# Kernel tuning notes

Measured on AMD Instinct MI355X. Metric: run time of the kernel, lower is better.

The kernel has to match this reference:

```python
import jax, jax.numpy as jnp
import numpy as np

B, S, D, H = 8, 1024, 768, 12
DH = D // H
EPS = 1e-5
NEG = -1e9


def _layernorm(x, g, b):
    mu = jnp.mean(x, axis=-1, keepdims=True)
    var = jnp.mean((x - mu) ** 2, axis=-1, keepdims=True)
    return (x - mu) * jax.lax.rsqrt(var + EPS) * g + b


def setup_inputs() -> dict:
    key = jax.random.key(0)
    ks = jax.random.split(key, 20)
    sc = 0.02
    x = jax.random.normal(ks[0], (B, S, D), dtype=jnp.float32)
    src_mask = jax.random.randint(ks[1], (B, S), 0, 2) > 0
    # weights stored as (in, out): y = x @ W + b (same math as torch x @ W.T + b)
    Wq = jax.random.normal(ks[2], (D, D), jnp.float32) * sc
    bq = jnp.zeros((D,), jnp.float32)
    Wk = jax.random.normal(ks[3], (D, D), jnp.float32) * sc
    bk = jnp.zeros((D,), jnp.float32)
    Wv = jax.random.normal(ks[4], (D, D), jnp.float32) * sc
    bv = jnp.zeros((D,), jnp.float32)
    Wo = jax.random.normal(ks[5], (D, D), jnp.float32) * sc
    bo = jnp.zeros((D,), jnp.float32)
    g1 = jnp.ones((D,), jnp.float32)
    be1 = jnp.zeros((D,), jnp.float32)
    W1 = jax.random.normal(ks[6], (D, 2 * D), jnp.float32) * sc
    b1 = jnp.zeros((2 * D,), jnp.float32)
    W2 = jax.random.normal(ks[7], (2 * D, D), jnp.float32) * sc
    b2 = jnp.zeros((D,), jnp.float32)
    g2 = jnp.ones((D,), jnp.float32)
    be2 = jnp.zeros((D,), jnp.float32)
    return dict(x=x, src_mask=src_mask, Wq=Wq, bq=bq, Wk=Wk, bk=bk, Wv=Wv, bv=bv,
                Wo=Wo, bo=bo, g1=g1, be1=be1, W1=W1, b1=b1, W2=W2, b2=b2,
                g2=g2, be2=be2)


def reference(x, src_mask, Wq, bq, Wk, bk, Wv, bv, Wo, bo, g1, be1, W1, b1, W2, b2, g2, be2):
    # QKV projections, split into heads: [B, S, H, DH]
    q = (x @ Wq + bq).reshape(B, S, H, DH)
    k = (x @ Wk + bk).reshape(B, S, H, DH)
    v = (x @ Wv + bv).reshape(B, S, H, DH)
    # scores [B, H, S, S]; scale by sqrt(head_dim) as in original
    scores = jnp.einsum('bqhd,bkhd->bhqk', q, k) / np.sqrt(DH).astype(np.float32)
    # additive key mask broadcast over heads and queries
    mask = jnp.where(src_mask[:, None, None, :], 0.0, NEG).astype(scores.dtype)
    A = jax.nn.softmax(scores + mask, axis=-1)
    ctx = jnp.einsum('bhqk,bkhd->bqhd', A, v).reshape(B, S, D)
    attn_out = ctx @ Wo + bo + x
    h = _layernorm(attn_out, g1, be1)
    ff = jax.nn.relu(h @ W1 + b1) @ W2 + b2
    out = _layernorm(ff + h, g2, be2)
    return out
```

## Files before the change

kernel.cpp:

```cpp
#include <hip/hip_runtime.h>
#include <cstdint>
#include <cstddef>

typedef unsigned short u16;
typedef __attribute__((ext_vector_type(8))) __bf16 bf16x8;
typedef __attribute__((ext_vector_type(4))) float floatx4;

#define Bz 8
#define Sz 1024
#define Dz 768
#define Hz 12
#define DHz 64

__device__ __forceinline__ u16 f2b(float f) {
  unsigned u = __float_as_uint(f);
  return (u16)((u + 0x7fffu + ((u >> 16) & 1u)) >> 16);
}

__device__ __forceinline__ bf16x8 ld8(const u16* p) {
  union { uint4 u; bf16x8 b; } t;
  t.u = *reinterpret_cast<const uint4*>(p);
  return t.b;
}

__device__ __forceinline__ void load_lds16(const u16* g, u16* l) {
  __builtin_amdgcn_global_load_lds(
      (const __attribute__((address_space(1))) unsigned int*)g,
      (__attribute__((address_space(3))) unsigned int*)l, 16, 0, 0);
}

__global__ __launch_bounds__(256) void cvt4(const float* __restrict__ src,
                                            u16* __restrict__ dst, int n4) {
  int i = blockIdx.x * 256 + threadIdx.x;
  if (i >= n4) return;
  float4 v = reinterpret_cast<const float4*>(src)[i];
  union { u16 s[4]; uint2 u; } t;
  t.s[0] = f2b(v.x); t.s[1] = f2b(v.y); t.s[2] = f2b(v.z); t.s[3] = f2b(v.w);
  reinterpret_cast<uint2*>(dst)[i] = t.u;
}

__global__ __launch_bounds__(256)
void wtrans(const float* __restrict__ s0, const float* __restrict__ s1,
            const float* __restrict__ s2, u16* __restrict__ dst,
            int K, int N, int srcN) {
  __shared__ float T[32][33];
  const int tx = threadIdx.x & 31, ty = threadIdx.x >> 5;
  const int n0 = blockIdx.x * 32, k0 = blockIdx.y * 32;
  const int n = n0 + tx;
  const float* src = s0;
  int nn = n;
  if (s1 && n >= 1536) { src = s2; nn = n - 1536; }
  else if (s1 && n >= 768) { src = s1; nn = n - 768; }
#pragma unroll
  for (int i = 0; i < 4; ++i)
    T[ty + i * 8][tx] = src[(size_t)(k0 + ty + i * 8) * srcN + nn];
  __syncthreads();
#pragma unroll
  for (int i = 0; i < 4; ++i)
    dst[(size_t)(n0 + ty + i * 8) * K + k0 + tx] = f2b(T[tx][ty + i * 8]);
}

template <int EPI>
__global__ __launch_bounds__(256, 3)
void gemm_k(const u16* __restrict__ A, const u16* __restrict__ Bt,
            int M, int N, int K,
            const float* __restrict__ bias0, const float* __restrict__ bias1,
            const float* __restrict__ bias2, const float* __restrict__ resid,
            float* __restrict__ outF, u16* __restrict__ outB,
            u16* __restrict__ qO, u16* __restrict__ kO, u16* __restrict__ vtO) {
  __shared__ __align__(16) u16 As[3][128 * 32];
  __shared__ __align__(16) u16 Bs[3][128 * 32];
  const int tid = threadIdx.x;
  const int lane = tid & 63, wave = tid >> 6;
  const int l15 = lane & 15, quad = lane >> 4;

  const int nx = gridDim.x;
  const int nwg = nx * gridDim.y;
  const int lin = blockIdx.y * nx + blockIdx.x;
  const int swz = (lin & 7) * (nwg >> 3) + (lin >> 3);
  const int bx = swz % nx, by = swz / nx;

  const int m0 = by * 128, n0 = bx * 128;
  const int wm = (wave >> 1) * 64, wn = (wave & 1) * 64;

  floatx4 acc[4][4];
#pragma unroll
  for (int i = 0; i < 4; ++i)
#pragma unroll
    for (int j = 0; j < 4; ++j) acc[i][j] = {0.f, 0.f, 0.f, 0.f};

  const int srow = lane >> 2;
  const int scol = (((lane & 3) ^ ((lane >> 3) & 3))) * 8;
  const u16* pA = A + (size_t)(m0 + wave * 32 + srow) * K + scol;
  const u16* pB = Bt + (size_t)(n0 + wave * 32 + srow) * K + scol;

#pragma unroll
  for (int t = 0; t < 2; ++t)
#pragma unroll
    for (int j = 0; j < 2; ++j) {
      load_lds16(pA + (size_t)(j * 16) * K + t * 32, &As[t][(wave * 2 + j) * 512]);
      load_lds16(pB + (size_t)(j * 16) * K + t * 32, &Bs[t][(wave * 2 + j) * 512]);
    }

  const int NIT = K >> 5;
  const int rsw = (l15 >> 1) & 3;
  int cur = 0;
  for (int i = 0; i < NIT; ++i) {
    if (i == NIT - 1) asm volatile("s_waitcnt vmcnt(0)" ::: "memory");
    else              asm volatile("s_waitcnt vmcnt(4)" ::: "memory");
    __builtin_amdgcn_s_barrier();
    bf16x8 af[4], bf[4];
#pragma unroll
    for (int ii = 0; ii < 4; ++ii)
      af[ii] = ld8(&As[cur][(wm + ii * 16 + l15) * 32 + (quad ^ rsw) * 8]);
#pragma unroll
    for (int j = 0; j < 4; ++j)
      bf[j] = ld8(&Bs[cur][(wn + j * 16 + l15) * 32 + (quad ^ rsw) * 8]);
    __builtin_amdgcn_sched_barrier(0);
    if (i + 2 < NIT) {
      const int k2 = (i + 2) << 5;
      int pf = cur + 2; if (pf >= 3) pf -= 3;
#pragma unroll
      for (int j = 0; j < 2; ++j) {
        load_lds16(pA + (size_t)(j * 16) * K + k2, &As[pf][(wave * 2 + j) * 512]);
        load_lds16(pB + (size_t)(j * 16) * K + k2, &Bs[pf][(wave * 2 + j) * 512]);
      }
    }
    __builtin_amdgcn_sched_barrier(0);
#pragma unroll
    for (int ii = 0; ii < 4; ++ii)
#pragma unroll
      for (int j = 0; j < 4; ++j)
        acc[ii][j] = __builtin_amdgcn_mfma_f32_16x16x32_bf16(af[ii], bf[j],
                                                             acc[ii][j], 0, 0, 0);
    cur += 1; if (cur == 3) cur = 0;
  }

#pragma unroll
  for (int i = 0; i < 4; ++i) {
    int mbase = m0 + wm + i * 16 + quad * 4;
#pragma unroll
    for (int j = 0; j < 4; ++j) {
      int n = n0 + wn + j * 16 + l15;
#pragma unroll
      for (int r = 0; r < 4; ++r) {
        int mm = mbase + r;
        float v = acc[i][j][r];
        if (EPI == 0) {
          if (n < 768) {
            v += bias0[n];
            qO[(size_t)mm * 768 + n] = f2b(v);
          } else if (n < 1536) {
            v += bias1[n - 768];
            kO[(size_t)mm * 768 + (n - 768)] = f2b(v);
          } else {
            int d = n - 1536;
            v += bias2[d];
            int hh = d >> 6, dh = d & 63;
            int bb = mm >> 10, ss = mm & 1023;
            vtO[((size_t)(bb * Hz + hh) * DHz + dh) * Sz + ss] = f2b(v);
          }
        } else if (EPI == 1) {
          v += bias0[n] + resid[(size_t)mm * N + n];
          outF[(size_t)mm * N + n] = v;
        } else {
          v += bias0[n];
          v = fmaxf(v, 0.f);
          outB[(size_t)mm * N + n] = f2b(v);
        }
      }
    }
  }
}

__global__ __launch_bounds__(256, 3)
void attn_k(const u16* __restrict__ q, const u16* __restrict__ kbuf,
            const u16* __restrict__ vt, const int* __restrict__ mask,
            u16* __restrict__ ctx) {
  __shared__ float addend[Sz];
  __shared__ __align__(16) u16 Ks[128 * 64];
  __shared__ __align__(16) u16 Vs[64 * 128];
  __shared__ __align__(16) u16 P[4][16][132];
  const int tid = threadIdx.x;
  const int wave = tid >> 6, lane = tid & 63;
  const int l15 = lane & 15, quad = lane >> 4;
  const int lin = blockIdx.y * 16 + blockIdx.x;
  const int swzid = (lin & 7) * 192 + (lin >> 3);
  const int bq = swzid & 15;
  const int bh = swzid >> 4;
  const int b = bh / Hz, h = bh - b * Hz;

  for (int s = tid; s < Sz; s += 256)
    addend[s] = mask[b * Sz + s] ? 0.f : -1e9f;

  const int qrow = bq * 64 + wave * 16 + l15;
  const u16* qp = q + (size_t)(b * Sz + qrow) * Dz + h * DHz;
  const bf16x8 fq0 = ld8(qp + quad * 8);
  const bf16x8 fq1 = ld8(qp + 32 + quad * 8);

  const int kchunk = (lane & 7) ^ (lane >> 3);
  const int l7 = l15 & 7;
  const int s0q = quad ^ l7;

  float m_l = -1e30f, l_l = 0.f;
  floatx4 o[4];
#pragma unroll
  for (int nt = 0; nt < 4; ++nt) o[nt] = {0.f, 0.f, 0.f, 0.f};

  const size_t vbase = (size_t)(b * Hz + h) * DHz * Sz;

  for (int kt = 0; kt < Sz / 128; ++kt) {
    __syncthreads();
#pragma unroll
    for (int j = 0; j < 4; ++j) {
      const int key = wave * 32 + j * 8 + (lane >> 3);
      load_lds16(kbuf + (size_t)(b * Sz + kt * 128 + key) * Dz + h * DHz +
                     kchunk * 8,
                 Ks + wave * 2048 + j * 512);
      const int dh = wave * 16 + j * 4 + (lane >> 4);
      const int vchunk = (lane & 15) ^ (dh & 7);
      load_lds16(vt + vbase + (size_t)dh * Sz + kt * 128 + vchunk * 8,
                 Vs + wave * 2048 + j * 512);
    }
    __syncthreads();

    floatx4 z[8];
#pragma unroll
    for (int t = 0; t < 8; ++t) {
      const int krow = t * 16 + l15;
      bf16x8 fk0 = ld8(&Ks[krow * 64 + s0q * 8]);
      bf16x8 fk1 = ld8(&Ks[krow * 64 + (s0q ^ 4) * 8]);
      floatx4 zz = {0.f, 0.f, 0.f, 0.f};
      zz = __builtin_amdgcn_mfma_f32_16x16x32_bf16(fk0, fq0, zz, 0, 0, 0);
      zz = __builtin_amdgcn_mfma_f32_16x16x32_bf16(fk1, fq1, zz, 0, 0, 0);
      const float4 ad =
          *reinterpret_cast<const float4*>(&addend[kt * 128 + t * 16 + quad * 4]);
      z[t][0] = zz[0] * 0.125f + ad.x;
      z[t][1] = zz[1] * 0.125f + ad.y;
      z[t][2] = zz[2] * 0.125f + ad.z;
      z[t][3] = zz[3] * 0.125f + ad.w;
    }
    float mx = z[0][0];
#pragma unroll
    for (int t = 0; t < 8; ++t)
#pragma unroll
      for (int r = 0; r < 4; ++r) mx = fmaxf(mx, z[t][r]);
    mx = fmaxf(mx, __shfl_xor(mx, 16, 64));
    mx = fmaxf(mx, __shfl_xor(mx, 32, 64));
    const float nm = fmaxf(m_l, mx);
    const float alpha = __expf(m_l - nm);
    m_l = nm;
    float su = 0.f;
#pragma unroll
    for (int t = 0; t < 8; ++t) {
      union { u16 s[4]; uint2 u; } pk;
#pragma unroll
      for (int r = 0; r < 4; ++r) {
        float p = __expf(z[t][r] - nm);
        su += p;
        pk.s[r] = f2b(p);
      }
      *reinterpret_cast<uint2*>(&P[wave][l15][t * 16 + quad * 4]) = pk.u;
    }
    su += __shfl_xor(su, 16, 64);
    su += __shfl_xor(su, 32, 64);
    l_l = l_l * alpha + su;
    float av[4];
#pragma unroll
    for (int r = 0; r < 4; ++r) av[r] = __shfl(alpha, quad * 4 + r, 64);
#pragma unroll
    for (int nt = 0; nt < 4; ++nt)
#pragma unroll
      for (int r = 0; r < 4; ++r) o[nt][r] *= av[r];
    bf16x8 ap[4];
#pragma unroll
    for (int c = 0; c < 4; ++c)
      ap[c] = ld8(&P[wave][l15][c * 32 + quad * 8]);
#pragma unroll
    for (int nt = 0; nt < 4; ++nt) {
#pragma unroll
      for (int c = 0; c < 4; ++c) {
        bf16x8 bv =
            ld8(&Vs[(nt * 16 + l15) * 128 + (((c * 4 + quad) ^ l7) * 8)]);
        o[nt] = __builtin_amdgcn_mfma_f32_16x16x32_bf16(ap[c], bv, o[nt], 0, 0, 0);
      }
    }
  }

  const float linv = 1.f / l_l;
  float lv[4];
#pragma unroll
  for (int r = 0; r < 4; ++r) lv[r] = __shfl(linv, quad * 4 + r, 64);
  const int qr = bq * 64 + wave * 16 + quad * 4;
#pragma unroll
  for (int nt = 0; nt < 4; ++nt)
#pragma unroll
    for (int r = 0; r < 4; ++r) {
      float v = o[nt][r] * lv[r];
      ctx[(size_t)(b * Sz + qr + r) * Dz + h * DHz + nt * 16 + l15] = f2b(v);
    }
}

__global__ __launch_bounds__(256)
void ln_k(const float* __restrict__ in, const float* __restrict__ g,
          const float* __restrict__ be, float* __restrict__ outF,
          u16* __restrict__ outB) {
  const int row = blockIdx.x;
  const float* x = in + (size_t)row * Dz;
  const int tid = threadIdx.x;
  float v0 = x[tid], v1 = x[tid + 256], v2 = x[tid + 512];
  float s = v0 + v1 + v2;
  float s2 = v0 * v0 + v1 * v1 + v2 * v2;
#pragma unroll
  for (int off = 1; off < 64; off <<= 1) {
    s += __shfl_xor(s, off, 64);
    s2 += __shfl_xor(s2, off, 64);
  }
  __shared__ float red[8];
  int wave = tid >> 6, lane = tid & 63;
  if (lane == 0) { red[wave] = s; red[4 + wave] = s2; }
  __syncthreads();
  s = red[0] + red[1] + red[2] + red[3];
  s2 = red[4] + red[5] + red[6] + red[7];
  const float mu = s * (1.f / 768.f);
  const float rstd = rsqrtf(s2 * (1.f / 768.f) - mu * mu + 1e-5f);
  float vv[3] = {v0, v1, v2};
#pragma unroll
  for (int e = 0; e < 3; ++e) {
    int col = tid + e * 256;
    float y = (vv[e] - mu) * rstd * g[col] + be[col];
    outF[(size_t)row * Dz + col] = y;
    if (outB) outB[(size_t)row * Dz + col] = f2b(y);
  }
}

extern "C" void kernel_launch(void* const* d_in, const int* in_sizes, int n_in,
                              void* d_out, int out_size, void* d_ws,
                              size_t ws_size, hipStream_t stream) {
  const float* x   = (const float*)d_in[0];
  const int*   msk = (const int*)d_in[1];
  const float* Wq  = (const float*)d_in[2];
  const float* bq  = (const float*)d_in[3];
  const float* Wk  = (const float*)d_in[4];
  const float* bk  = (const float*)d_in[5];
  const float* Wv  = (const float*)d_in[6];
  const float* bv  = (const float*)d_in[7];
  const float* Wo  = (const float*)d_in[8];
  const float* bo  = (const float*)d_in[9];
  const float* g1  = (const float*)d_in[10];
  const float* be1 = (const float*)d_in[11];
  const float* W1  = (const float*)d_in[12];
  const float* b1  = (const float*)d_in[13];
  const float* W2  = (const float*)d_in[14];
  const float* b2  = (const float*)d_in[15];
  const float* g2  = (const float*)d_in[16];
  const float* be2 = (const float*)d_in[17];
  float* out = (float*)d_out;

  char* ws = (char*)d_ws;
  u16*   xb    = (u16*)(ws + 0);
  u16*   wqkvb = (u16*)(ws + 12582912);
  u16*   wob   = (u16*)(ws + 16121856);
  u16*   w1b   = (u16*)(ws + 17301504);
  u16*   w2b   = (u16*)(ws + 19660800);
  u16*   qb    = (u16*)(ws + 22020096);
  u16*   kb    = (u16*)(ws + 34603008);
  u16*   vtb   = (u16*)(ws + 47185920);
  u16*   ctx   = (u16*)(ws + 59768832);
  float* att   = (float*)(ws + 72351744);
  float* hf    = (float*)(ws + 97517568);
  u16*   hb    = (u16*)(ws + 122683392);
  u16*   f1    = (u16*)(ws + 47185920);
  float* yy    = (float*)(ws + 22020096);

  cvt4<<<6291456 / 4 / 256, 256, 0, stream>>>(x, xb, 6291456 / 4);
  wtrans<<<dim3(2304 / 32, 768 / 32), 256, 0, stream>>>(Wq, Wk, Wv, wqkvb, 768,
                                                        2304, 768);
  wtrans<<<dim3(24, 24), 256, 0, stream>>>(Wo, nullptr, nullptr, wob, 768, 768,
                                           768);
  wtrans<<<dim3(48, 24), 256, 0, stream>>>(W1, nullptr, nullptr, w1b, 768, 1536,
                                           1536);
  wtrans<<<dim3(24, 48), 256, 0, stream>>>(W2, nullptr, nullptr, w2b, 1536, 768,
                                           768);

  gemm_k<0><<<dim3(2304 / 128, 8192 / 128), 256, 0, stream>>>(
      xb, wqkvb, 8192, 2304, 768, bq, bk, bv, nullptr, nullptr, nullptr, qb, kb,
      vtb);
  attn_k<<<dim3(Sz / 64, Bz * Hz), 256, 0, stream>>>(qb, kb, vtb, msk, ctx);
  gemm_k<1><<<dim3(768 / 128, 8192 / 128), 256, 0, stream>>>(
      ctx, wob, 8192, 768, 768, bo, nullptr, nullptr, x, att, nullptr, nullptr,
      nullptr, nullptr);
  ln_k<<<8192, 256, 0, stream>>>(att, g1, be1, hf, hb);
  gemm_k<2><<<dim3(1536 / 128, 8192 / 128), 256, 0, stream>>>(
      hb, w1b, 8192, 1536, 768, b1, nullptr, nullptr, nullptr, nullptr, f1,
      nullptr, nullptr, nullptr);
  gemm_k<1><<<dim3(768 / 128, 8192 / 128), 256, 0, stream>>>(
      f1, w2b, 8192, 768, 1536, b2, nullptr, nullptr, hf, yy, nullptr, nullptr,
      nullptr, nullptr);
  ln_k<<<8192, 256, 0, stream>>>(yy, g2, be2, out, nullptr);
}
```

Measured before the change: 368.8 us.

## Double-buffer K/V tiles in attention with lazy softmax rescaling

The attention kernel now uses 64-key tiles with double-buffered LDS for K and V. The next tile is prefetched with global_load_lds while the current one is computed, and a single barrier is used per iteration. The online softmax rescale is skipped unless the running max grows by more than a threshold, and the probabilities are packed to bf16 with the hardware conversion. This aims to hide global load latency and cut exp/shuffle/rescale work, at the cost of more loop iterations, reliance on manual vmcnt waits, and possible precision drift from the lazy max.

Result: faster. 357.8 us (-3.0%).

```diff
diff --git a/kernel.cpp b/kernel.cpp
--- a/kernel.cpp
+++ b/kernel.cpp
@@ -15,6 +15,11 @@
 __device__ __forceinline__ u16 f2b(float f) {
   unsigned u = __float_as_uint(f);
   return (u16)((u + 0x7fffu + ((u >> 16) & 1u)) >> 16);
+}
+
+__device__ __forceinline__ u16 f2b_hw(float f) {
+  __bf16 h = (__bf16)f;
+  return __builtin_bit_cast(u16, h);
 }
 
 __device__ __forceinline__ bf16x8 ld8(const u16* p) {
@@ -178,9 +183,9 @@
             const u16* __restrict__ vt, const int* __restrict__ mask,
             u16* __restrict__ ctx) {
   __shared__ float addend[Sz];
-  __shared__ __align__(16) u16 Ks[128 * 64];
-  __shared__ __align__(16) u16 Vs[64 * 128];
-  __shared__ __align__(16) u16 P[4][16][132];
+  __shared__ __align__(16) u16 Ks[2][64 * 64];
+  __shared__ __align__(16) u16 Vs[2][64 * 64];
+  __shared__ __align__(16) u16 P[4][16][68];
   const int tid = threadIdx.x;
   const int wave = tid >> 6, lane = tid & 63;
   const int l15 = lane & 15, quad = lane >> 4;
@@ -198,92 +203,104 @@
   const bf16x8 fq0 = ld8(qp + quad * 8);
   const bf16x8 fq1 = ld8(qp + 32 + quad * 8);
 
-  const int kchunk = (lane & 7) ^ (lane >> 3);
   const int l7 = l15 & 7;
   const int s0q = quad ^ l7;
 
+  const int srow = tid >> 3;
+  const int spos = tid & 7;
+  const int schunk = spos ^ (srow & 7);
+  const u16* kg = kbuf + (size_t)(b * Sz + srow) * Dz + h * DHz + schunk * 8;
+  const u16* vg = vt + (size_t)(b * Hz + h) * (DHz * Sz) + (size_t)srow * Sz +
+                  schunk * 8;
+
   float m_l = -1e30f, l_l = 0.f;
   floatx4 o[4];
 #pragma unroll
   for (int nt = 0; nt < 4; ++nt) o[nt] = {0.f, 0.f, 0.f, 0.f};
 
-  const size_t vbase = (size_t)(b * Hz + h) * DHz * Sz;
-
-  for (int kt = 0; kt < Sz / 128; ++kt) {
-    __syncthreads();
-#pragma unroll
-    for (int j = 0; j < 4; ++j) {
-      const int key = wave * 32 + j * 8 + (lane >> 3);
-      load_lds16(kbuf + (size_t)(b * Sz + kt * 128 + key) * Dz + h * DHz +
-                     kchunk * 8,
-                 Ks + wave * 2048 + j * 512);
-      const int dh = wave * 16 + j * 4 + (lane >> 4);
-      const int vchunk = (lane & 15) ^ (dh & 7);
-      load_lds16(vt + vbase + (size_t)dh * Sz + kt * 128 + vchunk * 8,
-                 Vs + wave * 2048 + j * 512);
-    }
-    __syncthreads();
-
-    floatx4 z[8];
-#pragma unroll
-    for (int t = 0; t < 8; ++t) {
+  load_lds16(kg, &Ks[0][wave * 512]);
+  load_lds16(kg + (size_t)32 * Dz, &Ks[0][2048 + wave * 512]);
+  load_lds16(vg, &Vs[0][wave * 512]);
+  load_lds16(vg + (size_t)32 * Sz, &Vs[0][2048 + wave * 512]);
+
+  for (int kt = 0; kt < 16; ++kt) {
+    const int cur = kt & 1;
+    asm volatile("s_waitcnt vmcnt(0)" ::: "memory");
+    __builtin_amdgcn_s_barrier();
+    bf16x8 fk0[4], fk1[4];
+#pragma unroll
+    for (int t = 0; t < 4; ++t) {
       const int krow = t * 16 + l15;
-      bf16x8 fk0 = ld8(&Ks[krow * 64 + s0q * 8]);
-      bf16x8 fk1 = ld8(&Ks[krow * 64 + (s0q ^ 4) * 8]);
+      fk0[t] = ld8(&Ks[cur][krow * 64 + s0q * 8]);
+      fk1[t] = ld8(&Ks[cur][krow * 64 + (s0q ^ 4) * 8]);
+    }
+    __builtin_amdgcn_sched_barrier(0);
+    if (kt + 1 < 16) {
+      const size_t ko = (size_t)(kt + 1) * 64 * Dz;
+      const int ve = (kt + 1) * 64;
+      const int nb = cur ^ 1;
+      load_lds16(kg + ko, &Ks[nb][wave * 512]);
+      load_lds16(kg + ko + (size_t)32 * Dz, &Ks[nb][2048 + wave * 512]);
+      load_lds16(vg + ve, &Vs[nb][wave * 512]);
+      load_lds16(vg + ve + (size_t)32 * Sz, &Vs[nb][2048 + wave * 512]);
+    }
+    __builtin_amdgcn_sched_barrier(0);
+
+    floatx4 z[4];
+#pragma unroll
+    for (int t = 0; t < 4; ++t) {
       floatx4 zz = {0.f, 0.f, 0.f, 0.f};
-      zz = __builtin_amdgcn_mfma_f32_16x16x32_bf16(fk0, fq0, zz, 0, 0, 0);
-      zz = __builtin_amdgcn_mfma_f32_16x16x32_bf16(fk1, fq1, zz, 0, 0, 0);
+      zz = __builtin_amdgcn_mfma_f32_16x16x32_bf16(fk0[t], fq0, zz, 0, 0, 0);
+      zz = __builtin_amdgcn_mfma_f32_16x16x32_bf16(fk1[t], fq1, zz, 0, 0, 0);
       const float4 ad =
-          *reinterpret_cast<const float4*>(&addend[kt * 128 + t * 16 + quad * 4]);
+          *reinterpret_cast<const float4*>(&addend[kt * 64 + t * 16 + quad * 4]);
       z[t][0] = zz[0] * 0.125f + ad.x;
       z[t][1] = zz[1] * 0.125f + ad.y;
       z[t][2] = zz[2] * 0.125f + ad.z;
       z[t][3] = zz[3] * 0.125f + ad.w;
     }
-    float mx = z[0][0];
-#pragma unroll
-    for (int t = 0; t < 8; ++t)
-#pragma unroll
-      for (int r = 0; r < 4; ++r) mx = fmaxf(mx, z[t][r]);
+    float mx = fmaxf(fmaxf(z[0][0], z[0][1]), fmaxf(z[0][2], z[0][3]));
+#pragma unroll
+    for (int t = 1; t < 4; ++t)
+      mx = fmaxf(mx, fmaxf(fmaxf(z[t][0], z[t][1]), fmaxf(z[t][2], z[t][3])));
     mx = fmaxf(mx, __shfl_xor(mx, 16, 64));
     mx = fmaxf(mx, __shfl_xor(mx, 32, 64));
-    const float nm = fmaxf(m_l, mx);
-    const float alpha = __expf(m_l - nm);
-    m_l = nm;
+    if (!__all(mx <= m_l + 8.f)) {
+      const float nm = fmaxf(m_l, mx);
+      const float alpha = __expf(m_l - nm);
+      m_l = nm;
+      l_l *= alpha;
+      float av[4];
+#pragma unroll
+      for (int r = 0; r < 4; ++r) av[r] = __shfl(alpha, quad * 4 + r, 64);
+#pragma unroll
+      for (int nt = 0; nt < 4; ++nt)
+#pragma unroll
+        for (int r = 0; r < 4; ++r) o[nt][r] *= av[r];
+    }
     float su = 0.f;
 #pragma unroll
-    for (int t = 0; t < 8; ++t) {
+    for (int t = 0; t < 4; ++t) {
       union { u16 s[4]; uint2 u; } pk;
 #pragma unroll
       for (int r = 0; r < 4; ++r) {
-        float p = __expf(z[t][r] - nm);
+        float p = __expf(z[t][r] - m_l);
         su += p;
-        pk.s[r] = f2b(p);
+        pk.s[r] = f2b_hw(p);
       }
       *reinterpret_cast<uint2*>(&P[wave][l15][t * 16 + quad * 4]) = pk.u;
     }
     su += __shfl_xor(su, 16, 64);
     su += __shfl_xor(su, 32, 64);
-    l_l = l_l * alpha + su;
-    float av[4];
-#pragma unroll
-    for (int r = 0; r < 4; ++r) av[r] = __shfl(alpha, quad * 4 + r, 64);
-#pragma unroll
-    for (int nt = 0; nt < 4; ++nt)
-#pragma unroll
-      for (int r = 0; r < 4; ++r) o[nt][r] *= av[r];
-    bf16x8 ap[4];
-#pragma unroll
-    for (int c = 0; c < 4; ++c)
-      ap[c] = ld8(&P[wave][l15][c * 32 + quad * 8]);
+    l_l += su;
+    const bf16x8 ap0 = ld8(&P[wave][l15][quad * 8]);
+    const bf16x8 ap1 = ld8(&P[wave][l15][32 + quad * 8]);
 #pragma unroll
     for (int nt = 0; nt < 4; ++nt) {
-#pragma unroll
-      for (int c = 0; c < 4; ++c) {
-        bf16x8 bv =
-            ld8(&Vs[(nt * 16 + l15) * 128 + (((c * 4 + quad) ^ l7) * 8)]);
-        o[nt] = __builtin_amdgcn_mfma_f32_16x16x32_bf16(ap[c], bv, o[nt], 0, 0, 0);
-      }
+      bf16x8 bv0 = ld8(&Vs[cur][(nt * 16 + l15) * 64 + ((quad ^ l7) * 8)]);
+      bf16x8 bv1 = ld8(&Vs[cur][(nt * 16 + l15) * 64 + (((4 + quad) ^ l7) * 8)]);
+      o[nt] = __builtin_amdgcn_mfma_f32_16x16x32_bf16(ap0, bv0, o[nt], 0, 0, 0);
+      o[nt] = __builtin_amdgcn_mfma_f32_16x16x32_bf16(ap1, bv1, o[nt], 0, 0, 0);
     }
   }
 
```
